# Kernel tuning notes

Measured on AMD Instinct MI355X. Metric: run time of the kernel, lower is better.

Reference implementation:

```python
import jax, jax.numpy as jnp
import numpy as np

D_MODEL = 768
NUM_HEADS = 12
D_K = D_MODEL // NUM_HEADS
WINDOW = 16
SPARSITY = 0.8
NEG = -1e9


def _pos_encoding(seq_len, d_model, dtype):
    pos = jnp.arange(seq_len, dtype=jnp.float32)[:, None]
    div = jnp.exp(jnp.arange(0, d_model, 2, dtype=jnp.float32) * (-np.log(10000.0) / d_model))
    pe = jnp.zeros((seq_len, d_model), dtype=jnp.float32)
    pe = pe.at[:, 0::2].set(jnp.sin(pos * div))
    pe = pe.at[:, 1::2].set(jnp.cos(pos * div))
    return pe.astype(dtype)


def _layernorm(x, gamma, beta, eps=1e-5):
    mu = jnp.mean(x, axis=-1, keepdims=True)
    var = jnp.mean(jnp.square(x - mu), axis=-1, keepdims=True)
    return (x - mu) * jax.lax.rsqrt(var + eps) * gamma + beta


def _split_heads(x):  # [B,S,D] -> [B,H,S,dk]
    b, s, _ = x.shape
    return x.reshape(b, s, NUM_HEADS, D_K).transpose(0, 2, 1, 3)


def _attn(q, k, v, mask):  # mask broadcastable to [B,H,S,S], bool
    scores = jnp.einsum('bhqd,bhkd->bhqk', q, k) / jnp.sqrt(jnp.asarray(D_K, q.dtype))
    scores = jnp.where(mask, scores, jnp.asarray(NEG, q.dtype))
    w = jax.nn.softmax(scores, axis=-1)
    out = jnp.einsum('bhqk,bhkd->bhqd', w, v)
    b, h, s, d = out.shape
    return out.transpose(0, 2, 1, 3).reshape(b, s, h * d)


def setup_inputs() -> dict:
    key = jax.random.key(0)
    ks = jax.random.split(key, 16)
    d = D_MODEL
    sc = 1.0 / np.sqrt(d)
    inp = {
        'x': jax.random.normal(ks[0], (2, 2048, d), jnp.float32),
        'wgq': jax.random.normal(ks[1], (d, d), jnp.float32) * sc,
        'wgk': jax.random.normal(ks[2], (d, d), jnp.float32) * sc,
        'wgv': jax.random.normal(ks[3], (d, d), jnp.float32) * sc,
        'wlq': jax.random.normal(ks[4], (d, d), jnp.float32) * sc,
        'wlk': jax.random.normal(ks[5], (d, d), jnp.float32) * sc,
        'wlv': jax.random.normal(ks[6], (d, d), jnp.float32) * sc,
        'wtq': jax.random.normal(ks[7], (d, d), jnp.float32) * sc,
        'wtk': jax.random.normal(ks[8], (d, d), jnp.float32) * sc,
        'wtv': jax.random.normal(ks[9], (d, d), jnp.float32) * sc,
        'w_out': jax.random.normal(ks[10], (3 * d, d), jnp.float32) * (1.0 / np.sqrt(3 * d)),
        'b_out': jnp.zeros((d,), jnp.float32),
        'w_gate': jax.random.normal(ks[11], (d, 3), jnp.float32) * sc,
        'b_gate': jnp.zeros((3,), jnp.float32),
        'w_sparse': jax.random.normal(ks[12], (d, 1), jnp.float32) * sc,
        'b_sparse': jnp.zeros((1,), jnp.float32),
        'g_gamma': jnp.ones((d,), jnp.float32), 'g_beta': jnp.zeros((d,), jnp.float32),
        'l_gamma': jnp.ones((d,), jnp.float32), 'l_beta': jnp.zeros((d,), jnp.float32),
        't_gamma': jnp.ones((d,), jnp.float32), 't_beta': jnp.zeros((d,), jnp.float32),
    }
    return inp


def reference(x, wgq, wgk, wgv, wlq, wlk, wlv, wtq, wtk, wtv,
              w_out, b_out, w_gate, b_gate, w_sparse, b_sparse,
              g_gamma, g_beta, l_gamma, l_beta, t_gamma, t_beta):
    b, s, d = x.shape
    # positional encoding branch input (dropout is identity at eval)
    x_pos = x + _pos_encoding(s, d, x.dtype)[None]

    # focus gate over mean-pooled tokens -> [B,3]
    fw = jax.nn.softmax(x.mean(axis=1) @ w_gate + b_gate, axis=-1)
    gw, lw, tw = fw[:, 0, None, None], fw[:, 1, None, None], fw[:, 2, None, None]

    # sparse (global) mask: keep top-k important columns per batch
    importance = (x @ w_sparse + b_sparse)[..., 0]  # [B,S]
    k = max(1, int((1.0 - SPARSITY) * s))
    _, topk_idx = jax.lax.top_k(importance, k)
    sparse = jnp.zeros((b, s), bool).at[jnp.arange(b)[:, None], topk_idx].set(True)
    sparse_mask = sparse[:, None, None, :]  # [B,1,1,S]

    idx = jnp.arange(s)
    rel = idx[None, :] - idx[:, None]
    half = WINDOW // 2
    local_mask = ((rel >= -half) & (rel <= half))[None, None]  # [1,1,S,S]

    stride = max(1, s // 8)
    temporal_cols = (idx % stride) == 0
    temporal_mask = jnp.broadcast_to(temporal_cols[None, :], (s, s))[None, None]

    # global branch
    g = _attn(_split_heads(x @ wgq), _split_heads(x @ wgk), _split_heads(x @ wgv), sparse_mask)
    g = _layernorm(g, g_gamma, g_beta)
    # local branch
    l = _attn(_split_heads(x @ wlq), _split_heads(x @ wlk), _split_heads(x @ wlv), local_mask)
    l = _layernorm(l, l_gamma, l_beta)
    # temporal branch (uses pos-encoded input)
    t = _attn(_split_heads(x_pos @ wtq), _split_heads(x_pos @ wtk), _split_heads(x_pos @ wtv), temporal_mask)
    t = _layernorm(t, t_gamma, t_beta)

    combined = jnp.concatenate([g * gw, l * lw, t * tw], axis=-1)
    return combined @ w_out + b_out
```

## Files before the change

kernel.cpp:

```cpp
#include <hip/hip_runtime.h>
#include <cstdint>

constexpr int BB   = 2;
constexpr int SS   = 2048;
constexpr int DD   = 768;
constexpr int HH   = 12;
constexpr int NTOK = BB * SS;
constexpr int KSEL = 409;
constexpr int KPAD = 448;
constexpr int NKT  = 7;

typedef __bf16 bf16x8 __attribute__((ext_vector_type(8)));
typedef float  f32x4  __attribute__((ext_vector_type(4)));

__device__ __forceinline__ float b2f(unsigned short u) {
  return __uint_as_float(((unsigned)u) << 16);
}
__device__ __forceinline__ unsigned short f2b(float f) {
  unsigned u = __float_as_uint(f);
  u += 0x7fffu + ((u >> 16) & 1u);
  return (unsigned short)(u >> 16);
}
__device__ __forceinline__ unsigned long long shfl_xor_u64(unsigned long long v, int m) {
  unsigned lo = (unsigned)v, hi = (unsigned)(v >> 32);
  lo = __shfl_xor(lo, m, 64);
  hi = __shfl_xor(hi, m, 64);
  return ((unsigned long long)hi << 32) | lo;
}

__device__ __forceinline__ void gload_lds16(const void* gsrc, void* ldst) {
  __builtin_amdgcn_global_load_lds(
      (__attribute__((address_space(1))) void*)(gsrc),
      (__attribute__((address_space(3))) void*)(ldst), 16, 0, 0);
}

__global__ __launch_bounds__(256) void mega_pre(
    const float* __restrict__ x, const float* __restrict__ wsp,
    const float* __restrict__ bsp,
    unsigned short* __restrict__ xb, unsigned short* __restrict__ xpb,
    float* __restrict__ imp,
    const float* w0, const float* w1, const float* w2, const float* w3,
    const float* w4, const float* w5, const float* w6, const float* w7,
    const float* w8, const float* w9,
    const float* __restrict__ gg, const float* __restrict__ lgam,
    const float* __restrict__ tg,
    const float* __restrict__ gb, const float* __restrict__ lbet,
    const float* __restrict__ tb,
    unsigned short* __restrict__ WTx4, unsigned short* __restrict__ WTkv,
    unsigned short* __restrict__ WTqt, unsigned short* __restrict__ WTtkv,
    unsigned short* __restrict__ WTo,
    float* __restrict__ Sbuf, float* __restrict__ Tbuf,
    float* __restrict__ partial) {
  __shared__ float tile[32][33];
  __shared__ float gsh[32], bsh[32];
  __shared__ float redS[8][32], redT[8][32];
  int id = blockIdx.x;
  int tid = threadIdx.x;

  if (id < SS) {
    int srow = id;
    const float* xr0 = x + (long)srow * DD;
    const float* xr1 = x + (long)(SS + srow) * DD;
    float acc0 = 0.f, acc1 = 0.f;
#pragma unroll
    for (int k = 0; k < 3; ++k) {
      int c = tid + k * 256;
      int j2 = c & ~1;
      float freq = __expf((float)j2 * -0.011992630692677323f);
      float ang = (float)srow * freq;
      float pe = (c & 1) ? cosf(ang) : sinf(ang);
      float w = wsp[c];
      float x0 = xr0[c], x1 = xr1[c];
      xb[(long)srow * DD + c]        = f2b(x0);
      xb[(long)(SS + srow) * DD + c] = f2b(x1);
      xpb[(long)srow * DD + c]        = f2b(x0 + pe);
      xpb[(long)(SS + srow) * DD + c] = f2b(x1 + pe);
      acc0 += x0 * w;
      acc1 += x1 * w;
    }
#pragma unroll
    for (int m = 1; m < 64; m <<= 1) {
      acc0 += __shfl_xor(acc0, m, 64);
      acc1 += __shfl_xor(acc1, m, 64);
    }
    __shared__ float red[8];
    int wv = tid >> 6, lane = tid & 63;
    if (lane == 0) { red[wv] = acc0; red[4 + wv] = acc1; }
    __syncthreads();
    if (tid == 0) {
      imp[srow]      = red[0] + red[1] + red[2] + red[3] + bsp[0];
      imp[SS + srow] = red[4] + red[5] + red[6] + red[7] + bsp[0];
    }
  } else if (id < SS + 6912) {
    int tidx = id - SS;
    int z, bx, by;
    if (tidx < 5184) { z = tidx / 576; int rem = tidx % 576; by = rem / 24; bx = rem % 24; }
    else             { z = 9; int rem = tidx - 5184; by = rem / 24; bx = rem % 24; }
    const float* srcs[10] = {w0, w1, w2, w3, w4, w5, w6, w7, w8, w9};
    const float* src = srcs[z];
    unsigned short* dst;
    int R = DD;
    switch (z) {
      case 0: dst = WTx4;                       break;
      case 1: dst = WTkv;                       break;
      case 2: dst = WTkv + (long)DD * DD;       break;
      case 3: dst = WTx4 + (long)DD * DD;       break;
      case 4: dst = WTx4 + (long)2 * DD * DD;   break;
      case 5: dst = WTx4 + (long)3 * DD * DD;   break;
      case 6: dst = WTqt;                       break;
      case 7: dst = WTtkv;                      break;
      case 8: dst = WTtkv + (long)DD * DD;      break;
      default: dst = WTo; R = 2304;             break;
    }
    int r0 = by * 32, c0 = bx * 32;
    int tx = tid & 31, ty = tid >> 5;
    for (int i = ty; i < 32; i += 8) tile[i][tx] = src[(long)(r0 + i) * DD + c0 + tx];
    if (z == 9 && ty == 0) {
      int kk = r0 + tx;
      gsh[tx] = (kk < 768) ? gg[kk] : (kk < 1536) ? lgam[kk - 768] : tg[kk - 1536];
      bsh[tx] = (kk < 768) ? gb[kk] : (kk < 1536) ? lbet[kk - 768] : tb[kk - 1536];
    }
    __syncthreads();
    if (z == 9) {
      float gamv = gsh[tx];
      for (int i = ty; i < 32; i += 8)
        dst[(long)(c0 + i) * R + r0 + tx] = f2b(tile[tx][i] * gamv);
      float pS = 0.f, pT = 0.f;
      for (int i = ty; i < 32; i += 8) {
        float wv = tile[i][tx];
        pS += gsh[i] * wv;
        pT += bsh[i] * wv;
      }
      redS[ty][tx] = pS; redT[ty][tx] = pT;
      __syncthreads();
      if (ty == 0) {
        float s = 0.f, t2 = 0.f;
#pragma unroll
        for (int j = 0; j < 8; ++j) { s += redS[j][tx]; t2 += redT[j][tx]; }
        int br = r0 / 768;
        atomicAdd(&Sbuf[br * DD + c0 + tx], s);
        atomicAdd(&Tbuf[br * DD + c0 + tx], t2);
      }
    } else {
      for (int i = ty; i < 32; i += 8)
        dst[(long)(c0 + i) * R + r0 + tx] = f2b(tile[tx][i]);
    }
  } else {
    int rem = id - SS - 6912;
    int chunk = rem & 15, b = rem >> 4;
    for (int c = tid; c < DD; c += 256) {
      const float* xp = x + ((long)(b * SS + chunk * 128)) * DD + c;
      float acc = 0.f;
      for (int s2 = 0; s2 < 128; ++s2) acc += xp[(long)s2 * DD];
      partial[(long)(b * 16 + chunk) * DD + c] = acc;
    }
  }
}

__global__ __launch_bounds__(1024) void topk_gate2(
    const float* __restrict__ imp, int* __restrict__ sel,
    const float* __restrict__ partial, const float* __restrict__ w_gate,
    const float* __restrict__ b_gate, float* __restrict__ fw) {
  int tid = threadIdx.x;
  if (blockIdx.x < 2) {
    __shared__ unsigned long long keys[SS];
    int b = blockIdx.x;
    for (int i = tid; i < SS; i += 1024) {
      float v = imp[b * SS + i];
      unsigned u = __float_as_uint(v);
      u = (u & 0x80000000u) ? ~u : (u | 0x80000000u);
      unsigned du = ~u;
      keys[i] = ((unsigned long long)du << 32) | (unsigned)i;
    }
    __syncthreads();
    for (int k = 2; k <= SS; k <<= 1) {
      for (int j = k >> 1; j >= 64; j >>= 1) {
        for (int i = tid; i < SS; i += 1024) {
          int p = i ^ j;
          if (p > i) {
            unsigned long long a = keys[i], bb = keys[p];
            bool up = ((i & k) == 0);
            if ((a > bb) == up) { keys[i] = bb; keys[p] = a; }
          }
        }
        __syncthreads();
      }
      unsigned long long k0 = keys[tid], k1 = keys[tid + 1024];
      bool up0 = ((tid & k) == 0);
      bool up1 = (((tid + 1024) & k) == 0);
      int j0 = (k >> 1) < 32 ? (k >> 1) : 32;
      for (int j = j0; j >= 1; j >>= 1) {
        bool low = ((tid & j) == 0);
        unsigned long long p0 = shfl_xor_u64(k0, j);
        k0 = ((low == up0) == (k0 < p0)) ? k0 : p0;
        unsigned long long p1 = shfl_xor_u64(k1, j);
        k1 = ((low == up1) == (k1 < p1)) ? k1 : p1;
      }
      keys[tid] = k0; keys[tid + 1024] = k1;
      __syncthreads();
    }
    for (int i = tid; i < KSEL; i += 1024) sel[b * KSEL + i] = (int)(keys[i] & 0xffffffffu);
  } else {
    __shared__ float meanbuf[DD];
    __shared__ float lg[3];
    int b = blockIdx.x - 2;
    if (tid < DD) {
      float acc = 0.f;
      for (int p = 0; p < 16; ++p) acc += partial[(long)(b * 16 + p) * DD + tid];
      meanbuf[tid] = acc * (1.0f / (float)SS);
    }
    __syncthreads();
    if (tid < 3) {
      float acc = b_gate[tid];
      for (int d = 0; d < DD; ++d) acc += meanbuf[d] * w_gate[d * 3 + tid];
      lg[tid] = acc;
    }
    __syncthreads();
    if (tid == 0) {
      float mx = fmaxf(lg[0], fmaxf(lg[1], lg[2]));
      float e0 = expf(lg[0] - mx), e1 = expf(lg[1] - mx), e2 = expf(lg[2] - mx);
      float inv = 1.f / (e0 + e1 + e2);
      fw[b * 3 + 0] = e0 * inv; fw[b * 3 + 1] = e1 * inv; fw[b * 3 + 2] = e2 * inv;
    }
  }
}

__global__ __launch_bounds__(256) void gemm_multi(
    const unsigned short* __restrict__ xb,    const unsigned short* __restrict__ WTx4,
    unsigned short* __restrict__ QKV4,
    const unsigned short* __restrict__ WTkv,  unsigned short* __restrict__ KVg,
    const unsigned short* __restrict__ xpb,   const unsigned short* __restrict__ WTqt,
    unsigned short* __restrict__ Qt,
    const unsigned short* __restrict__ WTtkv,
    const int* __restrict__ sel,
    unsigned short* __restrict__ K8, unsigned short* __restrict__ Vt8,
    unsigned short* __restrict__ Vt, unsigned short* __restrict__ Vtl) {
  __shared__ unsigned short AsB[2][4096];
  __shared__ unsigned short BsB[2][4096];
  constexpr int K = DD;
  const int tid = threadIdx.x;
  const int lane = tid & 63;
  const int wv = tid >> 6;
  const int wr = wv >> 1, wc = wv & 1;

  int lin = blockIdx.x;
  int xcd = lin & 7, idx = lin >> 3;
  const unsigned short* BT;
  int ntx, tile, region;
  if (idx < 96) {
    region = 0; BT = WTx4; ntx = 24;
    int r = (xcd >> 2) * 16 + (idx & 15);
    int c = (xcd & 3) * 6 + (idx >> 4);
    tile = r * 24 + c;
  } else {
    int e = xcd * 36 + (idx - 96);
    if (e < 84)       { region = 1; BT = WTkv;  ntx = 12; tile = e; }
    else if (e < 276) { region = 2; BT = WTqt;  ntx = 6;  tile = e - 84; }
    else              { region = 3; BT = WTtkv; ntx = 12; tile = e - 276; }
  }
  const long rowBase = (long)(tile / ntx) * 128;
  const long colBase = (long)(tile % ntx) * 128;

  auto arow = [&](int r) -> const unsigned short* {
    long grow = rowBase + r;
    if (region == 0) return xb + grow * (long)K;
    if (region == 2) return xpb + grow * (long)K;
    if (region == 1) {
      int bb2 = (int)(grow / KPAD), j = (int)(grow % KPAD);
      int srow = (j < KSEL) ? sel[bb2 * KSEL + j] : 0;
      return xb + ((long)bb2 * SS + srow) * (long)K;
    }
    if (grow < 16) {
      int bb2 = (int)grow >> 3, j = ((int)grow & 7) * 256;
      return xpb + ((long)bb2 * SS + j) * (long)K;
    }
    return xpb;
  };

  f32x4 acc[4][4];
#pragma unroll
  for (int i = 0; i < 4; ++i)
#pragma unroll
    for (int j = 0; j < 4; ++j)
#pragma unroll
      for (int r = 0; r < 4; ++r) acc[i][j][r] = 0.f;

  const int g0 = tid, g1 = tid + 256;
  const int r0 = g0 >> 2, k80 = (g0 & 3) ^ ((r0 >> 1) & 3);
  const int r1 = g1 >> 2, k81 = (g1 & 3) ^ ((r1 >> 1) & 3);
  const unsigned short* ga0 = arow(r0) + k80 * 8;
  const unsigned short* ga1 = arow(r1) + k81 * 8;
  const unsigned short* gb0 = BT + (colBase + r0) * (long)K + k80 * 8;
  const unsigned short* gb1 = BT + (colBase + r1) * (long)K + k81 * 8;

  const int k8 = lane >> 4;
  const int fr = lane & 15;
  int aoff[4], boff[4];
#pragma unroll
  for (int i = 0; i < 4; ++i) {
    int rowA = wr * 64 + i * 16 + fr;
    aoff[i] = (rowA * 4 + (k8 ^ ((rowA >> 1) & 3))) * 8;
    int rowB = wc * 64 + i * 16 + fr;
    boff[i] = (rowB * 4 + (k8 ^ ((rowB >> 1) & 3))) * 8;
  }

  auto stage = [&](int buf, int t) {
    int ko = t * 32;
    gload_lds16(ga0 + ko, &AsB[buf][g0 * 8]);
    gload_lds16(ga1 + ko, &AsB[buf][g1 * 8]);
    gload_lds16(gb0 + ko, &BsB[buf][g0 * 8]);
    gload_lds16(gb1 + ko, &BsB[buf][g1 * 8]);
  };

  constexpr int nk = K >> 5;
  stage(0, 0);
  __syncthreads();
  for (int t = 0; t < nk; ++t) {
    int cur = t & 1;
    if (t + 1 < nk) stage(cur ^ 1, t + 1);
    bf16x8 af[4], bfr[4];
#pragma unroll
    for (int i = 0; i < 4; ++i) af[i] = *(const bf16x8*)(&AsB[cur][aoff[i]]);
#pragma unroll
    for (int i = 0; i < 4; ++i) bfr[i] = *(const bf16x8*)(&BsB[cur][boff[i]]);
#pragma unroll
    for (int mi = 0; mi < 4; ++mi)
#pragma unroll
      for (int ni = 0; ni < 4; ++ni)
        acc[mi][ni] = __builtin_amdgcn_mfma_f32_16x16x32_bf16(af[mi], bfr[ni], acc[mi][ni], 0, 0, 0);
    __syncthreads();
  }

  int mode, vcol0 = 0, N = 0;
  unsigned short* C = nullptr;
  if (region == 0)      { mode = (colBase >= 2304) ? 1 : 0; C = QKV4; N = 3072;
                          vcol0 = (int)colBase - 2304; }
  else if (region == 1) { mode = (colBase >= 768) ? 2 : 0;  C = KVg;  N = 1536;
                          vcol0 = (int)colBase - 768; }
  else if (region == 2) { mode = 0; C = Qt; N = 768; }
  else                  { mode = (colBase >= 768) ? 4 : 3;
                          vcol0 = (int)colBase - 768; }

  const int orow0 = (lane >> 4) * 4;
  if (mode == 0) {
#pragma unroll
    for (int mi = 0; mi < 4; ++mi) {
      long gr = rowBase + wr * 64 + mi * 16 + orow0;
#pragma unroll
      for (int ni = 0; ni < 4; ++ni) {
        long gc = colBase + wc * 64 + ni * 16 + fr;
#pragma unroll
        for (int r = 0; r < 4; ++r)
          C[(gr + r) * (long)N + gc] = f2b(acc[mi][ni][r]);
      }
    }
  } else {
#pragma unroll
    for (int mi = 0; mi < 4; ++mi) {
      int lr = wr * 64 + mi * 16 + orow0;
      int grow = (int)rowBase + lr;
#pragma unroll
      for (int ni = 0; ni < 4; ++ni) {
        int lc = wc * 64 + ni * 16 + fr;
        uint2 pk;
        pk.x = (unsigned)f2b(acc[mi][ni][0]) | ((unsigned)f2b(acc[mi][ni][1]) << 16);
        pk.y = (unsigned)f2b(acc[mi][ni][2]) | ((unsigned)f2b(acc[mi][ni][3]) << 16);
        if (mode == 1) {
          int bb2 = grow >> 11, s = grow & (SS - 1);
          *(uint2*)(Vtl + ((long)bb2 * DD + vcol0 + lc) * SS + s) = pk;
        } else if (mode == 2) {
          int bb2 = grow / KPAD, j = grow - bb2 * KPAD;
          *(uint2*)(Vt + ((long)bb2 * DD + vcol0 + lc) * KPAD + j) = pk;
        } else if (mode == 3) {
          if (grow < 16) {
#pragma unroll
            for (int r = 0; r < 4; ++r) {
              int g2 = grow + r;
              K8[((long)(g2 >> 3) * 16 + (g2 & 7)) * DD + colBase + lc] =
                  f2b(acc[mi][ni][r]);
            }
          }
        } else {
          if (grow < 16) {
            *(uint2*)(Vt8 + ((long)(grow >> 3) * DD + vcol0 + lc) * 32 + (grow & 7)) = pk;
          }
        }
      }
    }
    if (mode == 4) {
#pragma unroll
      for (int e = 0; e < 6; ++e) {
        int id = tid + e * 256;
        int bb2 = id / 768, rem = id % 768;
        int c = rem / 6, ch = rem % 6;
        *(uint2*)(Vt8 + ((long)bb2 * DD + vcol0 + c) * 32 + 8 + ch * 4) = uint2{0u, 0u};
      }
    }
  }
}

__global__ __launch_bounds__(256) void gemm_final_sk(const unsigned short* __restrict__ A,
                                                     const unsigned short* __restrict__ BT,
                                                     float* __restrict__ Cpart) {
  __shared__ unsigned short As[2][128 * 32];
  __shared__ unsigned short Bs[2][128 * 32];
  constexpr int N = 768, K = 2304, CK = 768;
  const int tid = threadIdx.x;
  const int lane = tid & 63;
  const int wv = tid >> 6;
  const int wr = wv >> 1, wc = wv & 1;
  const int z = blockIdx.z;

  int lin = blockIdx.y * gridDim.x + blockIdx.x;
  int swz = (lin & 7) * 24 + (lin >> 3);
  const long rowBase = (long)(swz / 6) * 128;
  const long colBase = (long)(swz % 6) * 128;

  f32x4 acc[4][4];
#pragma unroll
  for (int i = 0; i < 4; ++i)
#pragma unroll
    for (int j = 0; j < 4; ++j)
#pragma unroll
      for (int r = 0; r < 4; ++r) acc[i][j][r] = 0.f;

  const int g0 = tid, g1 = tid + 256;
  const int r0 = g0 >> 2, k80 = (g0 & 3) ^ ((r0 >> 1) & 3);
  const int r1 = g1 >> 2, k81 = (g1 & 3) ^ ((r1 >> 1) & 3);
  const unsigned short* ga0 = A + (rowBase + r0) * (long)K + z * CK + k80 * 8;
  const unsigned short* ga1 = A + (rowBase + r1) * (long)K + z * CK + k81 * 8;
  const unsigned short* gb0 = BT + (colBase + r0) * (long)K + z * CK + k80 * 8;
  const unsigned short* gb1 = BT + (colBase + r1) * (long)K + z * CK + k81 * 8;

  const int k8 = lane >> 4;
  const int fr = lane & 15;
  int aoff[4], boff[4];
#pragma unroll
  for (int i = 0; i < 4; ++i) {
    int rowA = wr * 64 + i * 16 + fr;
    aoff[i] = (rowA * 4 + (k8 ^ ((rowA >> 1) & 3))) * 8;
    int rowB = wc * 64 + i * 16 + fr;
    boff[i] = (rowB * 4 + (k8 ^ ((rowB >> 1) & 3))) * 8;
  }

  auto stage = [&](int buf, int t) {
    int ko = t * 32;
    gload_lds16(ga0 + ko, &As[buf][g0 * 8]);
    gload_lds16(ga1 + ko, &As[buf][g1 * 8]);
    gload_lds16(gb0 + ko, &Bs[buf][g0 * 8]);
    gload_lds16(gb1 + ko, &Bs[buf][g1 * 8]);
  };

  constexpr int nk = CK >> 5;
  stage(0, 0);
  __syncthreads();
  for (int t = 0; t < nk; ++t) {
    int cur = t & 1;
    if (t + 1 < nk) stage(cur ^ 1, t + 1);
    bf16x8 af[4], bfr[4];
#pragma unroll
    for (int i = 0; i < 4; ++i) af[i] = *(const bf16x8*)(&As[cur][aoff[i]]);
#pragma unroll
    for (int i = 0; i < 4; ++i) bfr[i] = *(const bf16x8*)(&Bs[cur][boff[i]]);
#pragma unroll
    for (int mi = 0; mi < 4; ++mi)
#pragma unroll
      for (int ni = 0; ni < 4; ++ni)
        acc[mi][ni] = __builtin_amdgcn_mfma_f32_16x16x32_bf16(af[mi], bfr[ni], acc[mi][ni], 0, 0, 0);
    __syncthreads();
  }

  float* Cz = Cpart + (long)z * NTOK * DD;
  const int orow0 = (lane >> 4) * 4;
#pragma unroll
  for (int mi = 0; mi < 4; ++mi) {
    long gr = rowBase + wr * 64 + mi * 16 + orow0;
#pragma unroll
    for (int ni = 0; ni < 4; ++ni) {
      long gc = colBase + wc * 64 + ni * 16 + fr;
#pragma unroll
      for (int r = 0; r < 4; ++r)
        Cz[(gr + r) * (long)N + gc] = acc[mi][ni][r];
    }
  }
}

__global__ __launch_bounds__(256) void reduce_out(const float* __restrict__ P,
                                                  const float* __restrict__ bias,
                                                  const float* __restrict__ sumb,
                                                  const float* __restrict__ sqb,
                                                  const float* __restrict__ Sbuf,
                                                  const float* __restrict__ Tbuf,
                                                  const float* __restrict__ fw,
                                                  float* __restrict__ out) {
  long i = (long)blockIdx.x * 256 + threadIdx.x;
  int r = (int)(i / (DD / 4));
  int c4 = (int)(i % (DD / 4));
  int b = r >> 11;
  f32x4 o = *(const f32x4*)(bias + c4 * 4);
#pragma unroll
  for (int br = 0; br < 3; ++br) {
    float sum = sumb[br * NTOK + r];
    float sq  = sqb[br * NTOK + r];
    float mean = sum * (1.f / (float)DD);
    float var  = sq * (1.f / (float)DD) - mean * mean;
    float rs   = rsqrtf(var + 1e-5f);
    float gate = fw[b * 3 + br];
    f32x4 P4 = ((const f32x4*)(P + (long)br * NTOK * DD))[i];
    f32x4 S4 = *(const f32x4*)(Sbuf + br * DD + c4 * 4);
    f32x4 T4 = *(const f32x4*)(Tbuf + br * DD + c4 * 4);
#pragma unroll
    for (int e = 0; e < 4; ++e)
      o[e] += gate * (rs * (P4[e] - mean * S4[e]) + T4[e]);
  }
  ((f32x4*)out)[i] = o;
}

__device__ __forceinline__ void attn_flash_body(
    const unsigned short* __restrict__ QKV4,
    const unsigned short* __restrict__ KVg,
    const unsigned short* __restrict__ Vt,
    unsigned short* __restrict__ comb,
    float* __restrict__ sumb, float* __restrict__ sqb,
    unsigned short* smem) {
  unsigned short* Kl = smem;
  unsigned short* Vl = smem + 8192;
  unsigned short* Pl = smem + 16384;
  int tid = threadIdx.x, w = tid >> 6, lane = tid & 63;
  int fr = lane & 15, g = lane >> 4;
  int b = blockIdx.y / HH, h = blockIdx.y % HH, hoff = h * 64;
  int qbase = blockIdx.x * 64 + w * 16;
  long qrow = (long)b * SS + qbase + fr;

  const unsigned short* qptr = QKV4 + qrow * 3072 + hoff + g * 8;
  bf16x8 bq0 = *(const bf16x8*)(qptr);
  bf16x8 bq1 = *(const bf16x8*)(qptr + 32);

  const int s0 = tid, s1 = tid + 256;
  const int r0 = s0 >> 3, c0 = (s0 & 7) ^ (r0 & 7);
  const int r1 = s1 >> 3, c1 = (s1 & 7) ^ (r1 & 7);
  const unsigned short* kg_b = KVg + (long)b * KPAD * 1536 + hoff;
  const unsigned short* vt_b = Vt + ((long)b * DD + hoff) * KPAD;

  auto stage = [&](int buf, int t0) {
    gload_lds16(kg_b + (long)(t0 * 64 + r0) * 1536 + c0 * 8, &Kl[buf * 4096 + s0 * 8]);
    gload_lds16(kg_b + (long)(t0 * 64 + r1) * 1536 + c1 * 8, &Kl[buf * 4096 + s1 * 8]);
    gload_lds16(vt_b + (long)r0 * KPAD + t0 * 64 + c0 * 8, &Vl[buf * 4096 + s0 * 8]);
    gload_lds16(vt_b + (long)r1 * KPAD + t0 * 64 + c1 * 8, &Vl[buf * 4096 + s1 * 8]);
  };

  f32x4 oacc[4];
#pragma unroll
  for (int mf = 0; mf < 4; ++mf)
#pragma unroll
    for (int r = 0; r < 4; ++r) oacc[mf][r] = 0.f;
  float m = -3.0e38f, l = 0.f;

  stage(0, 0);
  asm volatile("s_waitcnt vmcnt(0)" ::: "memory");
  __syncthreads();

  for (int t = 0; t < NKT; ++t) {
    int cur = t & 1;
    if (t + 1 < NKT) stage(cur ^ 1, t + 1);

    f32x4 st[4];
#pragma unroll
    for (int kt = 0; kt < 4; ++kt) {
      int row = kt * 16 + fr;
      bf16x8 a0 = *(const bf16x8*)(&Kl[cur * 4096 + (row * 8 + (g ^ (row & 7))) * 8]);
      bf16x8 a1 = *(const bf16x8*)(&Kl[cur * 4096 + (row * 8 + ((4 + g) ^ (row & 7))) * 8]);
      f32x4 z = {0.f, 0.f, 0.f, 0.f};
      z = __builtin_amdgcn_mfma_f32_16x16x32_bf16(a0, bq0, z, 0, 0, 0);
      st[kt] = __builtin_amdgcn_mfma_f32_16x16x32_bf16(a1, bq1, z, 0, 0, 0);
    }

    float tm = -3.0e38f;
#pragma unroll
    for (int kt = 0; kt < 4; ++kt)
#pragma unroll
      for (int r = 0; r < 4; ++r) {
        int key = t * 64 + kt * 16 + g * 4 + r;
        float s = (key < KSEL) ? st[kt][r] * 0.125f : -1.0e30f;
        st[kt][r] = s;
        tm = fmaxf(tm, s);
      }
    tm = fmaxf(tm, __shfl_xor(tm, 16, 64));
    tm = fmaxf(tm, __shfl_xor(tm, 32, 64));
    float newm = fmaxf(m, tm);
    float f = __expf(m - newm);
    float tsum = 0.f;
#pragma unroll
    for (int kt = 0; kt < 4; ++kt)
#pragma unroll
      for (int r = 0; r < 4; ++r) {
        float e = __expf(st[kt][r] - newm);
        st[kt][r] = e;
        tsum += e;
      }
    tsum += __shfl_xor(tsum, 16, 64);
    tsum += __shfl_xor(tsum, 32, 64);
    l = l * f + tsum;
    m = newm;
#pragma unroll
    for (int mf = 0; mf < 4; ++mf)
#pragma unroll
      for (int r = 0; r < 4; ++r) oacc[mf][r] *= f;

    unsigned short* pw = &Pl[w * 1088 + fr * 68 + g * 4];
#pragma unroll
    for (int kt = 0; kt < 4; ++kt) {
      uint2 pk;
      pk.x = (unsigned)f2b(st[kt][0]) | ((unsigned)f2b(st[kt][1]) << 16);
      pk.y = (unsigned)f2b(st[kt][2]) | ((unsigned)f2b(st[kt][3]) << 16);
      *(uint2*)(pw + kt * 16) = pk;
    }

    const unsigned short* prd = &Pl[w * 1088 + fr * 68];
#pragma unroll
    for (int ks2 = 0; ks2 < 2; ++ks2) {
      bf16x8 pf = *(const bf16x8*)(prd + ks2 * 32 + g * 8);
#pragma unroll
      for (int mf = 0; mf < 4; ++mf) {
        int vr = mf * 16 + fr;
        int vc = ks2 * 4 + g;
        bf16x8 vf = *(const bf16x8*)(&Vl[cur * 4096 + (vr * 8 + (vc ^ (vr & 7))) * 8]);
        oacc[mf] = __builtin_amdgcn_mfma_f32_16x16x32_bf16(vf, pf, oacc[mf], 0, 0, 0);
      }
    }

    asm volatile("s_waitcnt vmcnt(0)" ::: "memory");
    __syncthreads();
  }

  float inv = 1.f / l;
  unsigned short* orow = comb + qrow * 2304 + hoff;
  float rsum = 0.f, rsq = 0.f;
#pragma unroll
  for (int mf = 0; mf < 4; ++mf) {
    float v0 = oacc[mf][0] * inv, v1 = oacc[mf][1] * inv;
    float v2 = oacc[mf][2] * inv, v3 = oacc[mf][3] * inv;
    rsum += v0 + v1 + v2 + v3;
    rsq  += v0 * v0 + v1 * v1 + v2 * v2 + v3 * v3;
    uint2 pk;
    pk.x = (unsigned)f2b(v0) | ((unsigned)f2b(v1) << 16);
    pk.y = (unsigned)f2b(v2) | ((unsigned)f2b(v3) << 16);
    *(uint2*)(orow + mf * 16 + g * 4) = pk;
  }
  rsum += __shfl_xor(rsum, 16, 64);
  rsum += __shfl_xor(rsum, 32, 64);
  rsq  += __shfl_xor(rsq, 16, 64);
  rsq  += __shfl_xor(rsq, 32, 64);
  if (lane < 16) {
    atomicAdd(&sumb[qrow], rsum);
    atomicAdd(&sqb[qrow], rsq);
  }
}

__device__ __forceinline__ void attn_win_body(
    const unsigned short* __restrict__ QKV,
    const unsigned short* __restrict__ K8,
    const unsigned short* __restrict__ Vt,
    unsigned short* __restrict__ comb, int brOff,
    float* __restrict__ sumb, float* __restrict__ sqb,
    int LD, int QO, long VSTR, bool local,
    unsigned short* smem) {
  int tid = threadIdx.x, w = tid >> 6, lane = tid & 63;
  int fr = lane & 15, g = lane >> 4;
  int b = blockIdx.y / HH, h = blockIdx.y % HH, hoff = h * 64;
  int qbase = blockIdx.x * 64 + w * 16;
  long qrow = (long)b * SS + qbase + fr;

  const unsigned short* qptr = QKV + qrow * LD + QO + hoff + g * 8;
  bf16x8 bq0 = *(const bf16x8*)(qptr);
  bf16x8 bq1 = *(const bf16x8*)(qptr + 32);

  int kstart = qbase - 8;
  if (kstart < 0) kstart = 0;
  if (kstart > SS - 32) kstart = SS - 32;

  f32x4 st[2];
  if (local) {
#pragma unroll
    for (int kt = 0; kt < 2; ++kt) {
      const unsigned short* kp =
          QKV + ((long)b * SS + kstart + kt * 16 + fr) * LD + 1536 + hoff + g * 8;
      bf16x8 a0 = *(const bf16x8*)(kp);
      bf16x8 a1 = *(const bf16x8*)(kp + 32);
      f32x4 z = {0.f, 0.f, 0.f, 0.f};
      z = __builtin_amdgcn_mfma_f32_16x16x32_bf16(a0, bq0, z, 0, 0, 0);
      st[kt] = __builtin_amdgcn_mfma_f32_16x16x32_bf16(a1, bq1, z, 0, 0, 0);
    }
  } else {
    const unsigned short* kp = K8 + ((long)b * 16 + fr) * DD + hoff + g * 8;
    bf16x8 a0 = *(const bf16x8*)(kp);
    bf16x8 a1 = *(const bf16x8*)(kp + 32);
    f32x4 z = {0.f, 0.f, 0.f, 0.f};
    z = __builtin_amdgcn_mfma_f32_16x16x32_bf16(a0, bq0, z, 0, 0, 0);
    st[0] = __builtin_amdgcn_mfma_f32_16x16x32_bf16(a1, bq1, z, 0, 0, 0);
    st[1] = f32x4{0.f, 0.f, 0.f, 0.f};
  }

  float m = -3.0e38f;
#pragma unroll
  for (int kt = 0; kt < 2; ++kt)
#pragma unroll
    for (int r = 0; r < 4; ++r) {
      int idx = kt * 16 + g * 4 + r;
      bool valid;
      if (local) {
        int rel = kstart + idx - qbase - fr;
        valid = (rel >= -8) && (rel <= 8);
      } else {
        valid = (idx < 8);
      }
      float s = valid ? st[kt][r] * 0.125f : -1.0e30f;
      st[kt][r] = s;
      m = fmaxf(m, s);
    }
  m = fmaxf(m, __shfl_xor(m, 16, 64));
  m = fmaxf(m, __shfl_xor(m, 32, 64));

  float lsum = 0.f;
#pragma unroll
  for (int kt = 0; kt < 2; ++kt)
#pragma unroll
    for (int r = 0; r < 4; ++r) {
      float e = __expf(st[kt][r] - m);
      st[kt][r] = e;
      lsum += e;
    }
  lsum += __shfl_xor(lsum, 16, 64);
  lsum += __shfl_xor(lsum, 32, 64);

  unsigned short* pl = smem + w * 640 + fr * 40 + g * 4;
#pragma unroll
  for (int kt = 0; kt < 2; ++kt) {
    uint2 pk;
    pk.x = (unsigned)f2b(st[kt][0]) | ((unsigned)f2b(st[kt][1]) << 16);
    pk.y = (unsigned)f2b(st[kt][2]) | ((unsigned)f2b(st[kt][3]) << 16);
    *(uint2*)(pl + kt * 16) = pk;
  }

  f32x4 oacc[4];
#pragma unroll
  for (int mf = 0; mf < 4; ++mf)
#pragma unroll
    for (int r = 0; r < 4; ++r) oacc[mf][r] = 0.f;

  const unsigned short* pr = smem + w * 640 + fr * 40 + g * 8;
  bf16x8 pf = *(const bf16x8*)(pr);
  long kb2 = local ? kstart : 0;
#pragma unroll
  for (int mf = 0; mf < 4; ++mf) {
    const unsigned short* vp =
        Vt + ((long)b * DD + hoff + mf * 16 + fr) * VSTR + kb2 + g * 8;
    bf16x8 vf = *(const bf16x8*)(vp);
    oacc[mf] = __builtin_amdgcn_mfma_f32_16x16x32_bf16(vf, pf, oacc[mf], 0, 0, 0);
  }

  float inv = 1.f / lsum;
  unsigned short* orow = comb + qrow * 2304 + brOff + hoff;
  float rsum = 0.f, rsq = 0.f;
#pragma unroll
  for (int mf = 0; mf < 4; ++mf) {
    float v0 = oacc[mf][0] * inv, v1 = oacc[mf][1] * inv;
    float v2 = oacc[mf][2] * inv, v3 = oacc[mf][3] * inv;
    rsum += v0 + v1 + v2 + v3;
    rsq  += v0 * v0 + v1 * v1 + v2 * v2 + v3 * v3;
    uint2 pk;
    pk.x = (unsigned)f2b(v0) | ((unsigned)f2b(v1) << 16);
    pk.y = (unsigned)f2b(v2) | ((unsigned)f2b(v3) << 16);
    *(uint2*)(orow + mf * 16 + g * 4) = pk;
  }
  rsum += __shfl_xor(rsum, 16, 64);
  rsum += __shfl_xor(rsum, 32, 64);
  rsq  += __shfl_xor(rsq, 16, 64);
  rsq  += __shfl_xor(rsq, 32, 64);
  if (lane < 16) {
    atomicAdd(&sumb[qrow], rsum);
    atomicAdd(&sqb[qrow], rsq);
  }
}

__global__ __launch_bounds__(256) void attn_all(
    const unsigned short* __restrict__ QKV4,
    const unsigned short* __restrict__ KVg,
    const unsigned short* __restrict__ Vt,
    const unsigned short* __restrict__ Qt,
    const unsigned short* __restrict__ K8,
    const unsigned short* __restrict__ Vt8,
    const unsigned short* __restrict__ Vtl,
    unsigned short* __restrict__ comb,
    float* __restrict__ sumb, float* __restrict__ sqb) {
  __shared__ unsigned short smem[20736];
  int z = blockIdx.z;
  if (z == 0) {
    attn_flash_body(QKV4, KVg, Vt, comb, sumb, sqb, smem);
  } else if (z == 1) {
    attn_win_body(QKV4, nullptr, Vtl, comb, 768, sumb + NTOK, sqb + NTOK,
                  3072, 768, SS, true, smem);
  } else {
    attn_win_body(Qt, K8, Vt8, comb, 1536, sumb + 2 * NTOK, sqb + 2 * NTOK,
                  768, 0, 32, false, smem);
  }
}

extern "C" void kernel_launch(void* const* d_in, const int* in_sizes, int n_in,
                              void* d_out, int out_size, void* d_ws, size_t ws_size,
                              hipStream_t stream) {
  const float* x        = (const float*)d_in[0];
  const float* wgq      = (const float*)d_in[1];
  const float* wgk      = (const float*)d_in[2];
  const float* wgv      = (const float*)d_in[3];
  const float* wlq      = (const float*)d_in[4];
  const float* wlk      = (const float*)d_in[5];
  const float* wlv      = (const float*)d_in[6];
  const float* wtq      = (const float*)d_in[7];
  const float* wtk      = (const float*)d_in[8];
  const float* wtv      = (const float*)d_in[9];
  const float* w_out    = (const float*)d_in[10];
  const float* b_out    = (const float*)d_in[11];
  const float* w_gate   = (const float*)d_in[12];
  const float* b_gate   = (const float*)d_in[13];
  const float* w_sparse = (const float*)d_in[14];
  const float* b_sparse = (const float*)d_in[15];
  const float* g_gamma  = (const float*)d_in[16];
  const float* g_beta   = (const float*)d_in[17];
  const float* l_gamma  = (const float*)d_in[18];
  const float* l_beta   = (const float*)d_in[19];
  const float* t_gamma  = (const float*)d_in[20];
  const float* t_beta   = (const float*)d_in[21];
  float* outp = (float*)d_out;

  unsigned short* xb    = (unsigned short*)d_ws;
  unsigned short* xpb   = xb    + (long)NTOK * DD;
  unsigned short* WTx4  = xpb   + (long)NTOK * DD;
  unsigned short* WTkv  = WTx4  + (long)3072 * DD;
  unsigned short* WTqt  = WTkv  + (long)1536 * DD;
  unsigned short* WTtkv = WTqt  + (long)DD * DD;
  unsigned short* WTo   = WTtkv + (long)1536 * DD;
  unsigned short* QKV4  = WTo   + (long)DD * 2304;
  unsigned short* Qt    = QKV4  + (long)NTOK * 3072;
  unsigned short* KVg   = Qt    + (long)NTOK * DD;
  unsigned short* K8    = KVg   + (long)BB * KPAD * 1536;
  unsigned short* Vt8   = K8    + (long)BB * 16 * DD;
  unsigned short* Vt    = Vt8   + (long)BB * DD * 32;
  unsigned short* Vtl   = Vt    + (long)BB * DD * KPAD;
  unsigned short* comb  = Vtl   + (long)BB * DD * SS;
  float* Cpart   = (float*)(comb + (long)NTOK * 2304);
  float* imp     = Cpart + 3L * NTOK * DD;
  float* partial = imp + NTOK;
  float* fw      = partial + 32 * DD;
  int*   sel     = (int*)(fw + 8);
  float* sumb    = (float*)(sel + 1024);
  float* sqb     = sumb + 3 * NTOK;
  float* Sbuf    = sqb + 3 * NTOK;
  float* Tbuf    = Sbuf + 3 * DD;

  hipMemsetAsync(sumb, 0, (size_t)(6 * NTOK + 6 * DD) * sizeof(float), stream);

  mega_pre<<<SS + 6912 + 32, 256, 0, stream>>>(
      x, w_sparse, b_sparse, xb, xpb, imp,
      wgq, wgk, wgv, wlq, wlk, wlv, wtq, wtk, wtv, w_out,
      g_gamma, l_gamma, t_gamma, g_beta, l_beta, t_beta,
      WTx4, WTkv, WTqt, WTtkv, WTo, Sbuf, Tbuf, partial);
  topk_gate2<<<4, 1024, 0, stream>>>(imp, sel, partial, w_gate, b_gate, fw);

  gemm_multi<<<1056, 256, 0, stream>>>(xb, WTx4, QKV4, WTkv, KVg,
                                       xpb, WTqt, Qt, WTtkv, sel,
                                       K8, Vt8, Vt, Vtl);

  attn_all<<<dim3(32, BB * HH, 3), 256, 0, stream>>>(QKV4, KVg, Vt, Qt, K8, Vt8,
                                                     Vtl, comb, sumb, sqb);

  gemm_final_sk<<<dim3(6, 32, 3), 256, 0, stream>>>(comb, WTo, Cpart);
  reduce_out<<<NTOK * DD / 4 / 256, 256, 0, stream>>>(Cpart, b_out, sumb, sqb,
                                                      Sbuf, Tbuf, fw, outp);
}
```

Before: 167.9 us.

## Overlap top-k sort with independent projection GEMMs in one fused launch

The top-k bitonic sort and the gate softmax move into the same launch as the projection GEMMs that do not depend on the selected indices. This hides the serial sort behind GEMM work, and only the sparse-gather KV GEMM stays in a separate launch after it. Because the blocks are launched with 1024 threads and three quarters of them exit at once, GEMM occupancy may drop under launch bounds of 1024, where register limits are tighter. The positional encoding also switches to the fast __sinf and __cosf intrinsics.

```diff
diff --git a/kernel.cpp b/kernel.cpp
--- a/kernel.cpp
+++ b/kernel.cpp
@@ -68,7 +68,7 @@
       int j2 = c & ~1;
       float freq = __expf((float)j2 * -0.011992630692677323f);
       float ang = (float)srow * freq;
-      float pe = (c & 1) ? cosf(ang) : sinf(ang);
+      float pe = (c & 1) ? __cosf(ang) : __sinf(ang);
       float w = wsp[c];
       float x0 = xr0[c], x1 = xr1[c];
       xb[(long)srow * DD + c]        = f2b(x0);
@@ -157,14 +157,175 @@
   }
 }
 
-__global__ __launch_bounds__(1024) void topk_gate2(
+__global__ __launch_bounds__(1024) void gemm_topk(
+    const unsigned short* __restrict__ xb,    const unsigned short* __restrict__ WTx4,
+    unsigned short* __restrict__ QKV4,
+    const unsigned short* __restrict__ xpb,   const unsigned short* __restrict__ WTqt,
+    unsigned short* __restrict__ Qt,
+    const unsigned short* __restrict__ WTtkv,
+    unsigned short* __restrict__ K8, unsigned short* __restrict__ Vt8,
+    unsigned short* __restrict__ Vtl,
     const float* __restrict__ imp, int* __restrict__ sel,
     const float* __restrict__ partial, const float* __restrict__ w_gate,
     const float* __restrict__ b_gate, float* __restrict__ fw) {
+  __shared__ unsigned long long smem_u64[4096];
+  int id = blockIdx.x;
   int tid = threadIdx.x;
-  if (blockIdx.x < 2) {
-    __shared__ unsigned long long keys[SS];
-    int b = blockIdx.x;
+
+  if (id < 972) {
+    if (tid >= 256) return;
+    unsigned short* AsB = (unsigned short*)smem_u64;
+    unsigned short* BsB = AsB + 8192;
+    constexpr int K = DD;
+    const int lane = tid & 63;
+    const int wv = tid >> 6;
+    const int wr = wv >> 1, wc = wv & 1;
+
+    const unsigned short* BT;
+    int ntx, tile, region;
+    if (id < 768) {
+      region = 0; BT = WTx4; ntx = 24;
+      int xcd = id & 7, idx = id >> 3;
+      int r = (xcd >> 2) * 16 + (idx & 15);
+      int c = (xcd & 3) * 6 + (idx >> 4);
+      tile = r * 24 + c;
+    } else {
+      int e = id - 768;
+      if (e < 192) { region = 2; BT = WTqt;  ntx = 6;  tile = e; }
+      else         { region = 3; BT = WTtkv; ntx = 12; tile = e - 192; }
+    }
+    const long rowBase = (long)(tile / ntx) * 128;
+    const long colBase = (long)(tile % ntx) * 128;
+
+    auto arow = [&](int r) -> const unsigned short* {
+      long grow = rowBase + r;
+      if (region == 0) return xb + grow * (long)K;
+      if (region == 2) return xpb + grow * (long)K;
+      if (grow < 16) {
+        int bb2 = (int)grow >> 3, j = ((int)grow & 7) * 256;
+        return xpb + ((long)bb2 * SS + j) * (long)K;
+      }
+      return xpb;
+    };
+
+    f32x4 acc[4][4];
+#pragma unroll
+    for (int i = 0; i < 4; ++i)
+#pragma unroll
+      for (int j = 0; j < 4; ++j)
+#pragma unroll
+        for (int r = 0; r < 4; ++r) acc[i][j][r] = 0.f;
+
+    const int g0 = tid, g1 = tid + 256;
+    const int r0 = g0 >> 2, k80 = (g0 & 3) ^ ((r0 >> 1) & 3);
+    const int r1 = g1 >> 2, k81 = (g1 & 3) ^ ((r1 >> 1) & 3);
+    const unsigned short* ga0 = arow(r0) + k80 * 8;
+    const unsigned short* ga1 = arow(r1) + k81 * 8;
+    const unsigned short* gb0 = BT + (colBase + r0) * (long)K + k80 * 8;
+    const unsigned short* gb1 = BT + (colBase + r1) * (long)K + k81 * 8;
+
+    const int k8 = lane >> 4;
+    const int fr = lane & 15;
+    int aoff[4], boff[4];
+#pragma unroll
+    for (int i = 0; i < 4; ++i) {
+      int rowA = wr * 64 + i * 16 + fr;
+      aoff[i] = (rowA * 4 + (k8 ^ ((rowA >> 1) & 3))) * 8;
+      int rowB = wc * 64 + i * 16 + fr;
+      boff[i] = (rowB * 4 + (k8 ^ ((rowB >> 1) & 3))) * 8;
+    }
+
+    auto stage = [&](int buf, int t) {
+      int ko = t * 32;
+      gload_lds16(ga0 + ko, &AsB[buf * 4096 + g0 * 8]);
+      gload_lds16(ga1 + ko, &AsB[buf * 4096 + g1 * 8]);
+      gload_lds16(gb0 + ko, &BsB[buf * 4096 + g0 * 8]);
+      gload_lds16(gb1 + ko, &BsB[buf * 4096 + g1 * 8]);
+    };
+
+    constexpr int nk = K >> 5;
+    stage(0, 0);
+    __syncthreads();
+    for (int t = 0; t < nk; ++t) {
+      int cur = t & 1;
+      if (t + 1 < nk) stage(cur ^ 1, t + 1);
+      bf16x8 af[4], bfr[4];
+#pragma unroll
+      for (int i = 0; i < 4; ++i) af[i] = *(const bf16x8*)(&AsB[cur * 4096 + aoff[i]]);
+#pragma unroll
+      for (int i = 0; i < 4; ++i) bfr[i] = *(const bf16x8*)(&BsB[cur * 4096 + boff[i]]);
+#pragma unroll
+      for (int mi = 0; mi < 4; ++mi)
+#pragma unroll
+        for (int ni = 0; ni < 4; ++ni)
+          acc[mi][ni] = __builtin_amdgcn_mfma_f32_16x16x32_bf16(af[mi], bfr[ni], acc[mi][ni], 0, 0, 0);
+      __syncthreads();
+    }
+
+    int mode, vcol0 = 0, N = 0;
+    unsigned short* C = nullptr;
+    if (region == 0)      { mode = (colBase >= 2304) ? 1 : 0; C = QKV4; N = 3072;
+                            vcol0 = (int)colBase - 2304; }
+    else if (region == 2) { mode = 0; C = Qt; N = 768; }
+    else                  { mode = (colBase >= 768) ? 4 : 3;
+                            vcol0 = (int)colBase - 768; }
+
+    const int orow0 = (lane >> 4) * 4;
+    if (mode == 0) {
+#pragma unroll
+      for (int mi = 0; mi < 4; ++mi) {
+        long gr = rowBase + wr * 64 + mi * 16 + orow0;
+#pragma unroll
+        for (int ni = 0; ni < 4; ++ni) {
+          long gc = colBase + wc * 64 + ni * 16 + fr;
+#pragma unroll
+          for (int r = 0; r < 4; ++r)
+            C[(gr + r) * (long)N + gc] = f2b(acc[mi][ni][r]);
+        }
+      }
+    } else {
+#pragma unroll
+      for (int mi = 0; mi < 4; ++mi) {
+        int lr = wr * 64 + mi * 16 + orow0;
+        int grow = (int)rowBase + lr;
+#pragma unroll
+        for (int ni = 0; ni < 4; ++ni) {
+          int lc = wc * 64 + ni * 16 + fr;
+          uint2 pk;
+          pk.x = (unsigned)f2b(acc[mi][ni][0]) | ((unsigned)f2b(acc[mi][ni][1]) << 16);
+          pk.y = (unsigned)f2b(acc[mi][ni][2]) | ((unsigned)f2b(acc[mi][ni][3]) << 16);
+          if (mode == 1) {
+            int bb2 = grow >> 11, s = grow & (SS - 1);
+            *(uint2*)(Vtl + ((long)bb2 * DD + vcol0 + lc) * SS + s) = pk;
+          } else if (mode == 3) {
+            if (grow < 16) {
+#pragma unroll
+              for (int r = 0; r < 4; ++r) {
+                int g2 = grow + r;
+                K8[((long)(g2 >> 3) * 16 + (g2 & 7)) * DD + colBase + lc] =
+                    f2b(acc[mi][ni][r]);
+              }
+            }
+          } else {
+            if (grow < 16) {
+              *(uint2*)(Vt8 + ((long)(grow >> 3) * DD + vcol0 + lc) * 32 + (grow & 7)) = pk;
+            }
+          }
+        }
+      }
+      if (mode == 4) {
+#pragma unroll
+        for (int e = 0; e < 6; ++e) {
+          int id2 = tid + e * 256;
+          int bb2 = id2 / 768, rem = id2 % 768;
+          int c = rem / 6, ch = rem % 6;
+          *(uint2*)(Vt8 + ((long)bb2 * DD + vcol0 + c) * 32 + 8 + ch * 4) = uint2{0u, 0u};
+        }
+      }
+    }
+  } else if (id < 974) {
+    unsigned long long* keys = smem_u64;
+    int b = id - 972;
     for (int i = tid; i < SS; i += 1024) {
       float v = imp[b * SS + i];
       unsigned u = __float_as_uint(v);
@@ -201,9 +362,9 @@
     }
     for (int i = tid; i < KSEL; i += 1024) sel[b * KSEL + i] = (int)(keys[i] & 0xffffffffu);
   } else {
-    __shared__ float meanbuf[DD];
-    __shared__ float lg[3];
-    int b = blockIdx.x - 2;
+    float* meanbuf = (float*)smem_u64;
+    float* lg = meanbuf + DD;
+    int b = id - 974;
     if (tid < DD) {
       float acc = 0.f;
       for (int p = 0; p < 16; ++p) acc += partial[(long)(b * 16 + p) * DD + tid];
@@ -225,16 +386,10 @@
   }
 }
 
-__global__ __launch_bounds__(256) void gemm_multi(
-    const unsigned short* __restrict__ xb,    const unsigned short* __restrict__ WTx4,
-    unsigned short* __restrict__ QKV4,
-    const unsigned short* __restrict__ WTkv,  unsigned short* __restrict__ KVg,
-    const unsigned short* __restrict__ xpb,   const unsigned short* __restrict__ WTqt,
-    unsigned short* __restrict__ Qt,
-    const unsigned short* __restrict__ WTtkv,
-    const int* __restrict__ sel,
-    unsigned short* __restrict__ K8, unsigned short* __restrict__ Vt8,
-    unsigned short* __restrict__ Vt, unsigned short* __restrict__ Vtl) {
+__global__ __launch_bounds__(256) void gemm_kvg(
+    const unsigned short* __restrict__ xb, const unsigned short* __restrict__ WTkv,
+    unsigned short* __restrict__ KVg, const int* __restrict__ sel,
+    unsigned short* __restrict__ Vt) {
   __shared__ unsigned short AsB[2][4096];
   __shared__ unsigned short BsB[2][4096];
   constexpr int K = DD;
@@ -243,38 +398,15 @@
   const int wv = tid >> 6;
   const int wr = wv >> 1, wc = wv & 1;
 
-  int lin = blockIdx.x;
-  int xcd = lin & 7, idx = lin >> 3;
-  const unsigned short* BT;
-  int ntx, tile, region;
-  if (idx < 96) {
-    region = 0; BT = WTx4; ntx = 24;
-    int r = (xcd >> 2) * 16 + (idx & 15);
-    int c = (xcd & 3) * 6 + (idx >> 4);
-    tile = r * 24 + c;
-  } else {
-    int e = xcd * 36 + (idx - 96);
-    if (e < 84)       { region = 1; BT = WTkv;  ntx = 12; tile = e; }
-    else if (e < 276) { region = 2; BT = WTqt;  ntx = 6;  tile = e - 84; }
-    else              { region = 3; BT = WTtkv; ntx = 12; tile = e - 276; }
-  }
-  const long rowBase = (long)(tile / ntx) * 128;
-  const long colBase = (long)(tile % ntx) * 128;
+  int tile = blockIdx.x;
+  const long rowBase = (long)(tile / 12) * 128;
+  const long colBase = (long)(tile % 12) * 128;
 
   auto arow = [&](int r) -> const unsigned short* {
     long grow = rowBase + r;
-    if (region == 0) return xb + grow * (long)K;
-    if (region == 2) return xpb + grow * (long)K;
-    if (region == 1) {
-      int bb2 = (int)(grow / KPAD), j = (int)(grow % KPAD);
-      int srow = (j < KSEL) ? sel[bb2 * KSEL + j] : 0;
-      return xb + ((long)bb2 * SS + srow) * (long)K;
-    }
-    if (grow < 16) {
-      int bb2 = (int)grow >> 3, j = ((int)grow & 7) * 256;
-      return xpb + ((long)bb2 * SS + j) * (long)K;
-    }
-    return xpb;
+    int bb2 = (int)(grow / KPAD), j = (int)(grow % KPAD);
+    int srow = (j < KSEL) ? sel[bb2 * KSEL + j] : 0;
+    return xb + ((long)bb2 * SS + srow) * (long)K;
   };
 
   f32x4 acc[4][4];
@@ -290,8 +422,8 @@
   const int r1 = g1 >> 2, k81 = (g1 & 3) ^ ((r1 >> 1) & 3);
   const unsigned short* ga0 = arow(r0) + k80 * 8;
   const unsigned short* ga1 = arow(r1) + k81 * 8;
-  const unsigned short* gb0 = BT + (colBase + r0) * (long)K + k80 * 8;
-  const unsigned short* gb1 = BT + (colBase + r1) * (long)K + k81 * 8;
+  const unsigned short* gb0 = WTkv + (colBase + r0) * (long)K + k80 * 8;
+  const unsigned short* gb1 = WTkv + (colBase + r1) * (long)K + k81 * 8;
 
   const int k8 = lane >> 4;
   const int fr = lane & 15;
@@ -331,18 +463,8 @@
     __syncthreads();
   }
 
-  int mode, vcol0 = 0, N = 0;
-  unsigned short* C = nullptr;
-  if (region == 0)      { mode = (colBase >= 2304) ? 1 : 0; C = QKV4; N = 3072;
-                          vcol0 = (int)colBase - 2304; }
-  else if (region == 1) { mode = (colBase >= 768) ? 2 : 0;  C = KVg;  N = 1536;
-                          vcol0 = (int)colBase - 768; }
-  else if (region == 2) { mode = 0; C = Qt; N = 768; }
-  else                  { mode = (colBase >= 768) ? 4 : 3;
-                          vcol0 = (int)colBase - 768; }
-
   const int orow0 = (lane >> 4) * 4;
-  if (mode == 0) {
+  if (colBase < 768) {
 #pragma unroll
     for (int mi = 0; mi < 4; ++mi) {
       long gr = rowBase + wr * 64 + mi * 16 + orow0;
@@ -351,49 +473,22 @@
         long gc = colBase + wc * 64 + ni * 16 + fr;
 #pragma unroll
         for (int r = 0; r < 4; ++r)
-          C[(gr + r) * (long)N + gc] = f2b(acc[mi][ni][r]);
+          KVg[(gr + r) * 1536L + gc] = f2b(acc[mi][ni][r]);
       }
     }
   } else {
+    int vcol0 = (int)colBase - 768;
 #pragma unroll
     for (int mi = 0; mi < 4; ++mi) {
-      int lr = wr * 64 + mi * 16 + orow0;
-      int grow = (int)rowBase + lr;
+      int grow = (int)rowBase + wr * 64 + mi * 16 + orow0;
+      int bb2 = grow / KPAD, j = grow - bb2 * KPAD;
 #pragma unroll
       for (int ni = 0; ni < 4; ++ni) {
         int lc = wc * 64 + ni * 16 + fr;
         uint2 pk;
         pk.x = (unsigned)f2b(acc[mi][ni][0]) | ((unsigned)f2b(acc[mi][ni][1]) << 16);
         pk.y = (unsigned)f2b(acc[mi][ni][2]) | ((unsigned)f2b(acc[mi][ni][3]) << 16);
-        if (mode == 1) {
-          int bb2 = grow >> 11, s = grow & (SS - 1);
-          *(uint2*)(Vtl + ((long)bb2 * DD + vcol0 + lc) * SS + s) = pk;
-        } else if (mode == 2) {
-          int bb2 = grow / KPAD, j = grow - bb2 * KPAD;
-          *(uint2*)(Vt + ((long)bb2 * DD + vcol0 + lc) * KPAD + j) = pk;
-        } else if (mode == 3) {
-          if (grow < 16) {
-#pragma unroll
-            for (int r = 0; r < 4; ++r) {
-              int g2 = grow + r;
-              K8[((long)(g2 >> 3) * 16 + (g2 & 7)) * DD + colBase + lc] =
-                  f2b(acc[mi][ni][r]);
-            }
-          }
-        } else {
-          if (grow < 16) {
-            *(uint2*)(Vt8 + ((long)(grow >> 3) * DD + vcol0 + lc) * 32 + (grow & 7)) = pk;
-          }
-        }
-      }
-    }
-    if (mode == 4) {
-#pragma unroll
-      for (int e = 0; e < 6; ++e) {
-        int id = tid + e * 256;
-        int bb2 = id / 768, rem = id % 768;
-        int c = rem / 6, ch = rem % 6;
-        *(uint2*)(Vt8 + ((long)bb2 * DD + vcol0 + c) * 32 + 8 + ch * 4) = uint2{0u, 0u};
+        *(uint2*)(Vt + ((long)bb2 * DD + vcol0 + lc) * KPAD + j) = pk;
       }
     }
   }
@@ -865,11 +960,11 @@
       wgq, wgk, wgv, wlq, wlk, wlv, wtq, wtk, wtv, w_out,
       g_gamma, l_gamma, t_gamma, g_beta, l_beta, t_beta,
       WTx4, WTkv, WTqt, WTtkv, WTo, Sbuf, Tbuf, partial);
-  topk_gate2<<<4, 1024, 0, stream>>>(imp, sel, partial, w_gate, b_gate, fw);
-
-  gemm_multi<<<1056, 256, 0, stream>>>(xb, WTx4, QKV4, WTkv, KVg,
-                                       xpb, WTqt, Qt, WTtkv, sel,
-                                       K8, Vt8, Vt, Vtl);
+
+  gemm_topk<<<976, 1024, 0, stream>>>(xb, WTx4, QKV4, xpb, WTqt, Qt, WTtkv,
+                                      K8, Vt8, Vtl, imp, sel,
+                                      partial, w_gate, b_gate, fw);
+  gemm_kvg<<<84, 256, 0, stream>>>(xb, WTkv, KVg, sel, Vt);
 
   attn_all<<<dim3(32, BB * HH, 3), 256, 0, stream>>>(QKV4, KVg, Vt, Qt, K8, Vt8,
                                                      Vtl, comb, sumb, sqb);
```

Result: slower. 181.3 us (+8.0%).

## Replace bitonic sort top-k with radix-select threshold and atomic compaction

Applied to the files above, without the earlier changes.

The full bitonic sort of 2048 64-bit keys used for top-k is replaced by an 8-bit-digit radix select that finds the k-th key, followed by an atomic compaction of every key at or below that threshold. The aim is to cut the many sort passes and barriers down to at most eight histogram passes. The selected indices now come out unordered, so anything downstream that relied on sorted order could change. The positional encoding also switches to fast __sinf/__cosf intrinsics, which lose accuracy for large angles.

```diff
diff --git a/kernel.cpp b/kernel.cpp
--- a/kernel.cpp
+++ b/kernel.cpp
@@ -20,12 +20,6 @@
   unsigned u = __float_as_uint(f);
   u += 0x7fffu + ((u >> 16) & 1u);
   return (unsigned short)(u >> 16);
-}
-__device__ __forceinline__ unsigned long long shfl_xor_u64(unsigned long long v, int m) {
-  unsigned lo = (unsigned)v, hi = (unsigned)(v >> 32);
-  lo = __shfl_xor(lo, m, 64);
-  hi = __shfl_xor(hi, m, 64);
-  return ((unsigned long long)hi << 32) | lo;
 }
 
 __device__ __forceinline__ void gload_lds16(const void* gsrc, void* ldst) {
@@ -68,7 +62,7 @@
       int j2 = c & ~1;
       float freq = __expf((float)j2 * -0.011992630692677323f);
       float ang = (float)srow * freq;
-      float pe = (c & 1) ? cosf(ang) : sinf(ang);
+      float pe = (c & 1) ? __cosf(ang) : __sinf(ang);
       float w = wsp[c];
       float x0 = xr0[c], x1 = xr1[c];
       xb[(long)srow * DD + c]        = f2b(x0);
@@ -163,43 +157,63 @@
     const float* __restrict__ b_gate, float* __restrict__ fw) {
   int tid = threadIdx.x;
   if (blockIdx.x < 2) {
-    __shared__ unsigned long long keys[SS];
+    __shared__ unsigned long long keybuf[SS];
+    __shared__ unsigned bins[256];
+    __shared__ unsigned long long prefix_s;
+    __shared__ unsigned long long Tsh;
+    __shared__ int need_s, done_s;
+    __shared__ unsigned cnt;
     int b = blockIdx.x;
     for (int i = tid; i < SS; i += 1024) {
       float v = imp[b * SS + i];
       unsigned u = __float_as_uint(v);
       u = (u & 0x80000000u) ? ~u : (u | 0x80000000u);
       unsigned du = ~u;
-      keys[i] = ((unsigned long long)du << 32) | (unsigned)i;
-    }
+      keybuf[i] = ((unsigned long long)du << 32) | (unsigned)i;
+    }
+    if (tid == 0) { prefix_s = 0ULL; need_s = KSEL; done_s = 0; cnt = 0; }
     __syncthreads();
-    for (int k = 2; k <= SS; k <<= 1) {
-      for (int j = k >> 1; j >= 64; j >>= 1) {
+
+    for (int shift = 56; shift >= 0; shift -= 8) {
+      unsigned long long himask = (shift == 56) ? 0ULL : (~0ULL << (shift + 8));
+      if (tid < 256) bins[tid] = 0;
+      __syncthreads();
+      for (int i = tid; i < SS; i += 1024) {
+        unsigned long long k = keybuf[i];
+        if ((k & himask) == prefix_s)
+          atomicAdd(&bins[(unsigned)((k >> shift) & 255ULL)], 1u);
+      }
+      __syncthreads();
+      if (tid == 0) {
+        unsigned cum = 0;
+        int d = 0;
+        for (; d < 255; ++d) {
+          if (cum + bins[d] >= (unsigned)need_s) break;
+          cum += bins[d];
+        }
+        prefix_s |= ((unsigned long long)(unsigned)d) << shift;
+        need_s -= (int)cum;
+        done_s = (bins[d] == 1 || shift == 0) ? 1 : 0;
+      }
+      __syncthreads();
+      if (done_s) {
+        unsigned long long smask = ~0ULL << shift;
         for (int i = tid; i < SS; i += 1024) {
-          int p = i ^ j;
-          if (p > i) {
-            unsigned long long a = keys[i], bb = keys[p];
-            bool up = ((i & k) == 0);
-            if ((a > bb) == up) { keys[i] = bb; keys[p] = a; }
-          }
+          unsigned long long k = keybuf[i];
+          if ((k & smask) == prefix_s) Tsh = k;
         }
         __syncthreads();
-      }
-      unsigned long long k0 = keys[tid], k1 = keys[tid + 1024];
-      bool up0 = ((tid & k) == 0);
-      bool up1 = (((tid + 1024) & k) == 0);
-      int j0 = (k >> 1) < 32 ? (k >> 1) : 32;
-      for (int j = j0; j >= 1; j >>= 1) {
-        bool low = ((tid & j) == 0);
-        unsigned long long p0 = shfl_xor_u64(k0, j);
-        k0 = ((low == up0) == (k0 < p0)) ? k0 : p0;
-        unsigned long long p1 = shfl_xor_u64(k1, j);
-        k1 = ((low == up1) == (k1 < p1)) ? k1 : p1;
-      }
-      keys[tid] = k0; keys[tid + 1024] = k1;
-      __syncthreads();
-    }
-    for (int i = tid; i < KSEL; i += 1024) sel[b * KSEL + i] = (int)(keys[i] & 0xffffffffu);
+        break;
+      }
+    }
+
+    unsigned long long T = Tsh;
+    for (int i = tid; i < SS; i += 1024) {
+      if (keybuf[i] <= T) {
+        unsigned p = atomicAdd(&cnt, 1u);
+        sel[b * KSEL + p] = (int)(keybuf[i] & 0xffffffffu);
+      }
+    }
   } else {
     __shared__ float meanbuf[DD];
     __shared__ float lg[3];
```

Result: slower. 172.5 us (+2.7%).
